# Kernel tuning notes

Hardware: AMD Instinct MI355X
Metric: run time of the kernel (lower is better)

## Reference

```python
import jax, jax.numpy as jnp
import numpy as np

N_NODES = 10000
N_EDGES = 160000
BN_EPS = 1e-5


def _sage(xx, src, dst, Wl, bl, Wr, n):
    # SAGEConv: lin_l(mean of in-neighbors) + lin_r(x)
    s = jax.ops.segment_sum(xx[src], dst, num_segments=n)
    cnt = jax.ops.segment_sum(jnp.ones((src.shape[0], 1), xx.dtype), dst, num_segments=n)
    mean = s / jnp.maximum(cnt, 1.0)
    return mean @ Wl + bl + xx @ Wr


def _gin(xx, src, dst, W1, b1, W2, b2, n):
    # GINConv (eps=0): MLP(x + sum of neighbors), MLP = Lin-ReLU-Lin-ReLU
    agg = xx + jax.ops.segment_sum(xx[src], dst, num_segments=n)
    h = jax.nn.relu(agg @ W1 + b1)
    return jax.nn.relu(h @ W2 + b2)


def _gat(xx, s2, d2, W, a_s, a_d, b, heads, ch, n):
    # GATConv with self-loops already appended in (s2, d2)
    h = (xx @ W).reshape(n, heads, ch)          # [N,H,C]
    al_s = (h * a_s).sum(-1)                     # [N,H]
    al_d = (h * a_d).sum(-1)                     # [N,H]
    e = jax.nn.leaky_relu(al_s[s2] + al_d[d2], negative_slope=0.2)  # [E',H]
    m = jax.ops.segment_max(e, d2, num_segments=n)
    ex = jnp.exp(e - m[d2])
    den = jax.ops.segment_sum(ex, d2, num_segments=n)
    coef = ex / den[d2]                          # segment softmax over dst
    out = jax.ops.segment_sum(h[s2] * coef[:, :, None], d2, num_segments=n)
    return out.reshape(n, heads * ch) + b


def reference(x, edge_index, train_edge_id,
              Wp1, bp1, Wp2, bp2, Wp3, bp3,
              sage1_Wl, sage1_bl, sage1_Wr, sage2_Wl, sage2_bl, sage2_Wr,
              gin1_W1, gin1_b1, gin1_W2, gin1_b2,
              gin2_W1, gin2_b1, gin2_W2, gin2_b2, gin_lin_W, gin_lin_b,
              gat1_W, gat1_as, gat1_ad, gat1_b,
              gat2_W, gat2_as, gat2_ad, gat2_b,
              fusion_w, lin1_W, lin1_b, lin2_W, lin2_b, fc2_W, fc2_b):
    n = x.shape[0]
    src, dst = edge_index[0], edge_index[1]
    # --- ppc: PointNet-style encoder: per-point MLP (16->64->128->256) + max pool over points ---
    pts = x[:, :, :16]                            # [N,L,16]
    h = jax.nn.relu(pts @ Wp1 + bp1)
    h = jax.nn.relu(h @ Wp2 + bp2)
    h = jax.nn.relu(h @ Wp3 + bp3)
    feat = h.max(axis=1)                          # [N,256]
    # --- SAGE branch ---
    hs = jax.nn.relu(_sage(feat, src, dst, sage1_Wl, sage1_bl, sage1_Wr, n))
    out_sage = _sage(hs, src, dst, sage2_Wl, sage2_bl, sage2_Wr, n)
    # --- GIN branch ---
    hg = jax.nn.relu(_gin(feat, src, dst, gin1_W1, gin1_b1, gin1_W2, gin1_b2, n))
    hg = jax.nn.relu(_gin(hg, src, dst, gin2_W1, gin2_b1, gin2_W2, gin2_b2, n))
    out_gin = hg @ gin_lin_W + gin_lin_b
    # --- GAT branch (self-loops per PyG default) ---
    loop = jnp.arange(n)
    s2 = jnp.concatenate([src, loop])
    d2 = jnp.concatenate([dst, loop])
    ha = jax.nn.relu(_gat(feat, s2, d2, gat1_W, gat1_as, gat1_ad, gat1_b, 8, 10, n))
    out_gat = _gat(ha, s2, d2, gat2_W, gat2_as, gat2_ad, gat2_b, 1, 512, n)
    # --- weighted fusion + batch norm (batch stats, no affine) ---
    y = fusion_w[0] * out_sage + fusion_w[1] * out_gin + fusion_w[2] * out_gat
    mu = y.mean(axis=0)
    var = y.var(axis=0)
    y = (y - mu) / jnp.sqrt(var + BN_EPS)
    # --- head ---
    y = jax.nn.relu(y @ lin1_W + lin1_b)
    y = y @ lin2_W + lin2_b
    # --- edge-pair gather + multiply for link scoring ---
    nid = edge_index[:, train_edge_id]            # [2,T]
    z = y[nid[0]] * y[nid[1]]
    return z @ fc2_W + fc2_b                      # [T,7]


def setup_inputs() -> dict:
    key = jax.random.key(0)
    ks = iter(jax.random.split(key, 64))
    def nrm(shape, s=0.02):
        return jax.random.normal(next(ks), shape, dtype=jnp.float32) * s
    inp = {}
    inp['x'] = jax.random.normal(next(ks), (N_NODES, 128, 16), dtype=jnp.float32)
    inp['edge_index'] = jax.random.randint(next(ks), (2, N_EDGES), 0, N_NODES, dtype=jnp.int32)
    inp['train_edge_id'] = jax.random.randint(next(ks), (50000,), 0, N_EDGES, dtype=jnp.int32)
    # ppc point encoder
    inp['Wp1'] = nrm((16, 64)); inp['bp1'] = nrm((64,))
    inp['Wp2'] = nrm((64, 128)); inp['bp2'] = nrm((128,))
    inp['Wp3'] = nrm((128, 256)); inp['bp3'] = nrm((256,))
    # SAGE: 256->128->512
    inp['sage1_Wl'] = nrm((256, 128)); inp['sage1_bl'] = nrm((128,)); inp['sage1_Wr'] = nrm((256, 128))
    inp['sage2_Wl'] = nrm((128, 512)); inp['sage2_bl'] = nrm((512,)); inp['sage2_Wr'] = nrm((128, 512))
    # GIN: 2 convs (256->128->128, 128->128->128) + lin 128->512
    inp['gin1_W1'] = nrm((256, 128)); inp['gin1_b1'] = nrm((128,))
    inp['gin1_W2'] = nrm((128, 128)); inp['gin1_b2'] = nrm((128,))
    inp['gin2_W1'] = nrm((128, 128)); inp['gin2_b1'] = nrm((128,))
    inp['gin2_W2'] = nrm((128, 128)); inp['gin2_b2'] = nrm((128,))
    inp['gin_lin_W'] = nrm((128, 512)); inp['gin_lin_b'] = nrm((512,))
    # GAT: layer1 256 -> 8 heads x 10 (concat=80), layer2 80 -> 512 (1 head)
    inp['gat1_W'] = nrm((256, 80)); inp['gat1_as'] = nrm((8, 10)); inp['gat1_ad'] = nrm((8, 10)); inp['gat1_b'] = nrm((80,))
    inp['gat2_W'] = nrm((80, 512)); inp['gat2_as'] = nrm((1, 512)); inp['gat2_ad'] = nrm((1, 512)); inp['gat2_b'] = nrm((512,))
    # fusion + head
    inp['fusion_w'] = jnp.ones((3,), jnp.float32)
    inp['lin1_W'] = nrm((512, 512)); inp['lin1_b'] = nrm((512,))
    inp['lin2_W'] = nrm((512, 512)); inp['lin2_b'] = nrm((512,))
    inp['fc2_W'] = nrm((512, 7)); inp['fc2_b'] = nrm((7,))
    return inp
```

## Files before the change

kernel.cpp:

```cpp
#include <hip/hip_runtime.h>
#include <math.h>

#define NN 10000
#define NE 160000
#define NT 50000

typedef unsigned short u16;
typedef unsigned int u32;
typedef __attribute__((ext_vector_type(8))) short bf16x8;
typedef __attribute__((ext_vector_type(4))) float f32x4;

__device__ __forceinline__ float bf2f(u16 u) { return __uint_as_float(((u32)u) << 16); }
__device__ __forceinline__ u16 f2bf(float f) {
    u32 x = __float_as_uint(f);
    return (u16)((x + 0x7fffu + ((x >> 16) & 1u)) >> 16);
}
__device__ __forceinline__ u32 cvtpk(float a, float b) {
    u32 r;
    asm("v_cvt_pk_bf16_f32 %0, %1, %2" : "=v"(r) : "v"(a), "v"(b));
    return r;
}
__device__ __forceinline__ float lrelu(float x) { return x > 0.f ? x : 0.2f * x; }

#define MFMA16(a, b, c) __builtin_amdgcn_mfma_f32_16x16x32_bf16((a), (b), (c), 0, 0, 0)

__global__ void k_wfrag(const float* __restrict__ W1, const float* __restrict__ W2,
                        const float* __restrict__ W3,
                        u16* __restrict__ W1f, u16* __restrict__ W2f, u16* __restrict__ W3f) {
    int i = blockIdx.x * 256 + threadIdx.x;
    if (i < 2048) {
        int e = i & 7, l = (i >> 3) & 63, nt = i >> 9;
        int k = (l >> 4) * 8 + e, c = nt * 16 + (l & 15);
        W1f[i] = (k < 16) ? f2bf(W1[k * 64 + c]) : (u16)0;
    }
    if (i < 8192) {
        int e = i & 7, l = (i >> 3) & 63, nt = (i >> 9) & 7, ks = i >> 12;
        int k = ks * 32 + (l >> 4) * 8 + e, c = nt * 16 + (l & 15);
        W2f[i] = f2bf(W2[k * 128 + c]);
    }
    if (i < 32768) {
        int e = i & 7, l = (i >> 3) & 63, nt = (i >> 9) & 15, ks = i >> 13;
        int k = ks * 32 + (l >> 4) * 8 + e, c = nt * 16 + (l & 15);
        W3f[i] = f2bf(W3[k * 256 + c]);
    }
}

__global__ void k_pack(const float* __restrict__ W, u16* __restrict__ Wf, int K, int Mt) {
    int total = (((K + 63) & ~63) >> 5) * Mt * 512;
    for (int i = blockIdx.x * 256 + threadIdx.x; i < total; i += gridDim.x * 256) {
        int e = i & 7, l = (i >> 3) & 63, mt = (i >> 9) % Mt, kk = i / (Mt << 9);
        int k = (kk << 5) + ((l >> 4) << 3) + e;
        int c = (mt << 4) + (l & 15);
        Wf[i] = (k < K) ? f2bf(W[(size_t)k * (Mt << 4) + c]) : (u16)0;
    }
}

__global__ __launch_bounds__(256) void k_pointnet_mfma(
    const float* __restrict__ x,
    const u16* __restrict__ W1f, const float* __restrict__ b1,
    const u16* __restrict__ W2f, const float* __restrict__ b2,
    const u16* __restrict__ W3f, const float* __restrict__ b3,
    u16* __restrict__ featb)
{
    __shared__ u16 buf[16384];

    const int node = blockIdx.x;
    const int t = threadIdx.x;
    const int w = t >> 6;
    const int l = t & 63;
    const int lr = l & 15;
    const int lg = l >> 4;

    {
        union { u32 q[4]; bf16x8 v; } ua0, ua1;
        ua0.q[0] = ua0.q[1] = ua0.q[2] = ua0.q[3] = 0;
        ua1 = ua0;
        if (lg < 2) {
            const float* px = x + ((size_t)node * 128 + w * 32 + lr) * 16 + lg * 8;
            float4 f0 = *(const float4*)px;
            float4 f1 = *(const float4*)(px + 4);
            ua0.q[0] = cvtpk(f0.x, f0.y); ua0.q[1] = cvtpk(f0.z, f0.w);
            ua0.q[2] = cvtpk(f1.x, f1.y); ua0.q[3] = cvtpk(f1.z, f1.w);
            float4 g0 = *(const float4*)(px + 256);
            float4 g1 = *(const float4*)(px + 260);
            ua1.q[0] = cvtpk(g0.x, g0.y); ua1.q[1] = cvtpk(g0.z, g0.w);
            ua1.q[2] = cvtpk(g1.x, g1.y); ua1.q[3] = cvtpk(g1.z, g1.w);
        }
        f32x4 acc[2][4];
        #pragma unroll
        for (int nt = 0; nt < 4; ++nt) {
            float bv = b1[nt * 16 + lr];
            f32x4 ci = {bv, bv, bv, bv};
            bf16x8 bf_ = *(const bf16x8*)(W1f + (nt * 64 + l) * 8);
            acc[0][nt] = MFMA16(ua0.v, bf_, ci);
            acc[1][nt] = MFMA16(ua1.v, bf_, ci);
        }
        #pragma unroll
        for (int mt = 0; mt < 2; ++mt) {
            #pragma unroll
            for (int nt = 0; nt < 4; ++nt) {
                int col = nt * 16 + lr;
                int r0 = w * 32 + mt * 16 + lg * 4;
                u32 p01 = cvtpk(fmaxf(acc[mt][nt][0], 0.f), fmaxf(acc[mt][nt][1], 0.f));
                u32 p23 = cvtpk(fmaxf(acc[mt][nt][2], 0.f), fmaxf(acc[mt][nt][3], 0.f));
                buf[((r0    ) * 64 + col) ^ (((r0    ) & 7) << 3)] = (u16)p01;
                buf[((r0 + 1) * 64 + col) ^ (((r0 + 1) & 7) << 3)] = (u16)(p01 >> 16);
                buf[((r0 + 2) * 64 + col) ^ (((r0 + 2) & 7) << 3)] = (u16)p23;
                buf[((r0 + 3) * 64 + col) ^ (((r0 + 3) & 7) << 3)] = (u16)(p23 >> 16);
            }
        }
    }

    {
        bf16x8 af[2][2];
        #pragma unroll
        for (int mt = 0; mt < 2; ++mt) {
            #pragma unroll
            for (int ks = 0; ks < 2; ++ks) {
                int row = w * 32 + mt * 16 + lr;
                int elem = row * 64 + ks * 32 + lg * 8;
                af[mt][ks] = *(const bf16x8*)&buf[elem ^ ((row & 7) << 3)];
            }
        }
        __syncthreads();

        f32x4 acc2[2][8];
        #pragma unroll
        for (int nt = 0; nt < 8; ++nt) {
            float bv = b2[nt * 16 + lr];
            f32x4 ci = {bv, bv, bv, bv};
            acc2[0][nt] = ci;
            acc2[1][nt] = ci;
        }
        #pragma unroll
        for (int ks = 0; ks < 2; ++ks) {
            #pragma unroll
            for (int nt = 0; nt < 8; ++nt) {
                bf16x8 bf_ = *(const bf16x8*)(W2f + ((ks * 8 + nt) * 64 + l) * 8);
                acc2[0][nt] = MFMA16(af[0][ks], bf_, acc2[0][nt]);
                acc2[1][nt] = MFMA16(af[1][ks], bf_, acc2[1][nt]);
            }
        }
        #pragma unroll
        for (int mt = 0; mt < 2; ++mt) {
            #pragma unroll
            for (int nt = 0; nt < 8; ++nt) {
                int col = nt * 16 + lr;
                int r0 = w * 32 + mt * 16 + lg * 4;
                u32 p01 = cvtpk(fmaxf(acc2[mt][nt][0], 0.f), fmaxf(acc2[mt][nt][1], 0.f));
                u32 p23 = cvtpk(fmaxf(acc2[mt][nt][2], 0.f), fmaxf(acc2[mt][nt][3], 0.f));
                buf[((r0    ) * 128 + col) ^ (((r0    ) & 7) << 3)] = (u16)p01;
                buf[((r0 + 1) * 128 + col) ^ (((r0 + 1) & 7) << 3)] = (u16)(p01 >> 16);
                buf[((r0 + 2) * 128 + col) ^ (((r0 + 2) & 7) << 3)] = (u16)p23;
                buf[((r0 + 3) * 128 + col) ^ (((r0 + 3) & 7) << 3)] = (u16)(p23 >> 16);
            }
        }
    }
    __syncthreads();

    {
        float pmax[4] = {0.f, 0.f, 0.f, 0.f};
        #pragma unroll
        for (int half = 0; half < 2; ++half) {
            f32x4 acc3[4][4];
            #pragma unroll
            for (int nt = 0; nt < 4; ++nt) {
                float bv = b3[w * 64 + nt * 16 + lr];
                f32x4 ci = {bv, bv, bv, bv};
                #pragma unroll
                for (int mt = 0; mt < 4; ++mt) acc3[mt][nt] = ci;
            }
            #pragma unroll
            for (int ks = 0; ks < 4; ++ks) {
                bf16x8 bf_[4];
                #pragma unroll
                for (int nt = 0; nt < 4; ++nt)
                    bf_[nt] = *(const bf16x8*)(W3f + ((ks * 16 + w * 4 + nt) * 64 + l) * 8);
                #pragma unroll
                for (int mt = 0; mt < 4; ++mt) {
                    int row = half * 64 + mt * 16 + lr;
                    int elem = row * 128 + ks * 32 + lg * 8;
                    bf16x8 af = *(const bf16x8*)&buf[elem ^ ((row & 7) << 3)];
                    #pragma unroll
                    for (int nt = 0; nt < 4; ++nt)
                        acc3[mt][nt] = MFMA16(af, bf_[nt], acc3[mt][nt]);
                }
            }
            #pragma unroll
            for (int nt = 0; nt < 4; ++nt) {
                #pragma unroll
                for (int mt = 0; mt < 4; ++mt) {
                    pmax[nt] = fmaxf(fmaxf(pmax[nt], acc3[mt][nt][0]),
                                     fmaxf(acc3[mt][nt][1],
                                           fmaxf(acc3[mt][nt][2], acc3[mt][nt][3])));
                }
            }
        }
        #pragma unroll
        for (int nt = 0; nt < 4; ++nt) {
            pmax[nt] = fmaxf(pmax[nt], __shfl_xor(pmax[nt], 16));
            pmax[nt] = fmaxf(pmax[nt], __shfl_xor(pmax[nt], 32));
        }
        if (l < 16) {
            #pragma unroll
            for (int nt = 0; nt < 4; ++nt)
                featb[(size_t)node * 256 + w * 64 + nt * 16 + l] = f2bf(pmax[nt]);
        }
    }
}

template<int CT, int DUAL, int RELU, int OUTM, int NORMA>
__global__ __launch_bounds__(256) void k_mm(
    const u16* __restrict__ A, const u16* __restrict__ A2,
    const u16* __restrict__ Bf, const u16* __restrict__ B2f,
    const float* __restrict__ bias, int K, int Mt,
    void* __restrict__ outp,
    const float* __restrict__ scale_ptr, int scale_idx,
    const float* __restrict__ mu, const float* __restrict__ inv)
{
    __shared__ u16 As[8192];
    __shared__ u16 As2[DUAL ? 8192 : 8];

    const int t = threadIdx.x;
    const int l = t & 63, lr = l & 15, lg = l >> 4;
    const int row0 = blockIdx.y << 7;
    const int ct0 = blockIdx.x * CT;
    const int m0 = (t >> 6) << 5;

    f32x4 acc[2][CT];
    #pragma unroll
    for (int nt = 0; nt < CT; ++nt) {
        float bv = bias ? bias[((ct0 + nt) << 4) + lr] : 0.f;
        f32x4 ci = {bv, bv, bv, bv};
        acc[0][nt] = ci;
        acc[1][nt] = ci;
    }

    const int KS = (K + 63) >> 6;
    for (int kblk = 0; kblk < KS; ++kblk) {
        const int k0 = kblk << 6;
        if (kblk) __syncthreads();
        #pragma unroll
        for (int j = 0; j < 4; ++j) {
            int si = t + (j << 8);
            int row = si >> 3, seg = si & 7;
            int gr = row0 + row;
            int kb = k0 + (seg << 3);
            int soff = ((row << 6) + (seg << 3)) ^ ((row & 7) << 3);
            if (NORMA) {
                u32 q0 = 0, q1 = 0, q2 = 0, q3 = 0;
                if (gr < NN) {
                    const float* Af = (const float*)A;
                    float4 f0 = *(const float4*)(Af + (size_t)gr * K + kb);
                    float4 f1 = *(const float4*)(Af + (size_t)gr * K + kb + 4);
                    q0 = cvtpk((f0.x - mu[kb+0]) * inv[kb+0], (f0.y - mu[kb+1]) * inv[kb+1]);
                    q1 = cvtpk((f0.z - mu[kb+2]) * inv[kb+2], (f0.w - mu[kb+3]) * inv[kb+3]);
                    q2 = cvtpk((f1.x - mu[kb+4]) * inv[kb+4], (f1.y - mu[kb+5]) * inv[kb+5]);
                    q3 = cvtpk((f1.z - mu[kb+6]) * inv[kb+6], (f1.w - mu[kb+7]) * inv[kb+7]);
                }
                u32* dst = (u32*)&As[soff];
                dst[0] = q0; dst[1] = q1; dst[2] = q2; dst[3] = q3;
            } else {
                bf16x8 v = {0,0,0,0,0,0,0,0};
                bf16x8 v2 = {0,0,0,0,0,0,0,0};
                if (gr < NN) {
                    if (kb + 8 <= K) {
                        v = *(const bf16x8*)(A + (size_t)gr * K + kb);
                        if (DUAL) v2 = *(const bf16x8*)(A2 + (size_t)gr * K + kb);
                    } else {
                        #pragma unroll
                        for (int e = 0; e < 8; ++e) if (kb + e < K) {
                            v[e] = (short)A[(size_t)gr * K + kb + e];
                            if (DUAL) v2[e] = (short)A2[(size_t)gr * K + kb + e];
                        }
                    }
                }
                *(bf16x8*)&As[soff] = v;
                if (DUAL) *(bf16x8*)&As2[soff] = v2;
            }
        }
        __syncthreads();
        #pragma unroll
        for (int ks = 0; ks < 2; ++ks) {
            const int kk = (k0 >> 5) + ks;
            bf16x8 bfr[CT];
            #pragma unroll
            for (int nt = 0; nt < CT; ++nt)
                bfr[nt] = *(const bf16x8*)(Bf + (((size_t)kk * Mt + ct0 + nt) << 9) + (l << 3));
            #pragma unroll
            for (int mt = 0; mt < 2; ++mt) {
                int row = m0 + (mt << 4) + lr;
                int soff = ((row << 6) + (ks << 5) + (lg << 3)) ^ ((row & 7) << 3);
                bf16x8 af = *(const bf16x8*)&As[soff];
                #pragma unroll
                for (int nt = 0; nt < CT; ++nt)
                    acc[mt][nt] = MFMA16(af, bfr[nt], acc[mt][nt]);
            }
            if (DUAL) {
                bf16x8 bfr2[CT];
                #pragma unroll
                for (int nt = 0; nt < CT; ++nt)
                    bfr2[nt] = *(const bf16x8*)(B2f + (((size_t)kk * Mt + ct0 + nt) << 9) + (l << 3));
                #pragma unroll
                for (int mt = 0; mt < 2; ++mt) {
                    int row = m0 + (mt << 4) + lr;
                    int soff = ((row << 6) + (ks << 5) + (lg << 3)) ^ ((row & 7) << 3);
                    bf16x8 af2 = *(const bf16x8*)&As2[soff];
                    #pragma unroll
                    for (int nt = 0; nt < CT; ++nt)
                        acc[mt][nt] = MFMA16(af2, bfr2[nt], acc[mt][nt]);
                }
            }
        }
    }

    float scale = 1.f;
    if (OUTM == 1 || OUTM == 2) scale = scale_ptr[scale_idx];
    const int M = Mt << 4;
    #pragma unroll
    for (int mt = 0; mt < 2; ++mt) {
        #pragma unroll
        for (int nt = 0; nt < CT; ++nt) {
            int col = ((ct0 + nt) << 4) + lr;
            #pragma unroll
            for (int r = 0; r < 4; ++r) {
                int grow = row0 + m0 + (mt << 4) + (lg << 2) + r;
                if (grow >= NN) continue;
                float v = acc[mt][nt][r];
                if (RELU) v = fmaxf(v, 0.f);
                size_t o = (size_t)grow * M + col;
                if (OUTM == 0) ((u16*)outp)[o] = f2bf(v);
                else if (OUTM == 1) ((float*)outp)[o] = scale * v;
                else if (OUTM == 2) ((float*)outp)[o] += scale * v;
                else ((float*)outp)[o] = v;
            }
        }
    }
}

__global__ void k_init(int* counts, float* s1, float* s2) {
    int i = blockIdx.x * 256 + threadIdx.x;
    if (i < NN) counts[i] = 0;
    if (i < 512) { s1[i] = 0.f; s2[i] = 0.f; }
}

__global__ void k_csr_count(const int* __restrict__ EI, int* counts) {
    int e = blockIdx.x * 256 + threadIdx.x;
    if (e < NE) atomicAdd(&counts[EI[NE + e]], 1);
}

__global__ __launch_bounds__(1024) void k_scan(const int* __restrict__ counts,
                                               int* offs, int* cursor) {
    __shared__ int buf[1024];
    int t = threadIdx.x;
    int carry = 0;
    for (int chunk = 0; chunk < (NN + 1023) / 1024; ++chunk) {
        int i = chunk * 1024 + t;
        int v = (i < NN) ? counts[i] : 0;
        buf[t] = v;
        __syncthreads();
        for (int o = 1; o < 1024; o <<= 1) {
            int xv = (t >= o) ? buf[t - o] : 0;
            __syncthreads();
            buf[t] += xv;
            __syncthreads();
        }
        int excl = buf[t] - v;
        if (i < NN) { offs[i] = carry + excl; cursor[i] = carry + excl; }
        carry += buf[1023];
        __syncthreads();
    }
    if (t == 0) offs[NN] = carry;
}

__global__ void k_csr_scatter(const int* __restrict__ EI, int* cursor, int* csrc) {
    int e = blockIdx.x * 256 + threadIdx.x;
    if (e < NE) {
        int d = EI[NE + e];
        int pos = atomicAdd(&cursor[d], 1);
        csrc[pos] = EI[e];
    }
}

template<int WU, int MODE>
__global__ void k_aggb(const u32* __restrict__ in, u32* __restrict__ out,
                       const int* __restrict__ offs, const int* __restrict__ srcs)
{
    int node = blockIdx.x;
    int c = threadIdx.x;
    int o0 = offs[node], o1 = offs[node + 1];
    float s0 = 0.f, s1 = 0.f;
    for (int j = o0; j < o1; ++j) {
        u32 v = in[(size_t)srcs[j] * WU + c];
        s0 += bf2f((u16)(v & 0xffff));
        s1 += bf2f((u16)(v >> 16));
    }
    if (MODE == 0) {
        int d = o1 - o0;
        float r = 1.f / (float)(d > 0 ? d : 1);
        s0 *= r; s1 *= r;
    } else {
        u32 v = in[(size_t)node * WU + c];
        s0 += bf2f((u16)(v & 0xffff));
        s1 += bf2f((u16)(v >> 16));
    }
    out[(size_t)node * WU + c] = cvtpk(s0, s1);
}

__global__ void k_gat1_al(const u16* __restrict__ h, const float* __restrict__ a_s,
                          const float* __restrict__ a_d, float* als, float* ald) {
    int idx = blockIdx.x * 64 + threadIdx.x;
    if (idx >= NN * 8) return;
    int node = idx >> 3, hh = idx & 7;
    float s = 0.f, d = 0.f;
    #pragma unroll
    for (int c = 0; c < 10; ++c) {
        float hv = bf2f(h[node * 80 + hh * 10 + c]);
        s = fmaf(hv, a_s[hh * 10 + c], s);
        d = fmaf(hv, a_d[hh * 10 + c], d);
    }
    als[idx] = s; ald[idx] = d;
}

__global__ __launch_bounds__(128) void k_gat1_attn(
    const u16* __restrict__ h, const float* __restrict__ als,
    const float* __restrict__ ald, const float* __restrict__ bias,
    const int* __restrict__ offs, const int* __restrict__ srcs,
    u16* __restrict__ ha)
{
    int node = blockIdx.x;
    int t = threadIdx.x;
    if (t >= 80) return;
    int hh = t / 10;
    int o0 = offs[node], o1 = offs[node + 1];
    float ad = ald[node * 8 + hh];
    float eself = lrelu(als[node * 8 + hh] + ad);
    float m = eself;
    for (int j = o0; j < o1; ++j)
        m = fmaxf(m, lrelu(als[srcs[j] * 8 + hh] + ad));
    float den = 0.f, num = 0.f;
    {
        float wgt = __expf(eself - m);
        den += wgt; num += wgt * bf2f(h[(size_t)node * 80 + t]);
    }
    for (int j = o0; j < o1; ++j) {
        int sc = srcs[j];
        float wgt = __expf(lrelu(als[sc * 8 + hh] + ad) - m);
        den += wgt; num += wgt * bf2f(h[(size_t)sc * 80 + t]);
    }
    ha[(size_t)node * 80 + t] = f2bf(fmaxf(num / den + bias[t], 0.f));
}

__global__ __launch_bounds__(256) void k_gat2_al(
    const u16* __restrict__ h, const float* __restrict__ a_s,
    const float* __restrict__ a_d, float* als, float* ald)
{
    __shared__ float rs[256], rd[256];
    int node = blockIdx.x, t = threadIdx.x;
    float h0 = bf2f(h[(size_t)node * 512 + t]);
    float h1 = bf2f(h[(size_t)node * 512 + 256 + t]);
    rs[t] = h0 * a_s[t] + h1 * a_s[256 + t];
    rd[t] = h0 * a_d[t] + h1 * a_d[256 + t];
    __syncthreads();
    for (int o = 128; o > 0; o >>= 1) {
        if (t < o) { rs[t] += rs[t + o]; rd[t] += rd[t + o]; }
        __syncthreads();
    }
    if (t == 0) { als[node] = rs[0]; ald[node] = rd[0]; }
}

__global__ __launch_bounds__(256) void k_gat2_attn(
    const u16* __restrict__ h, const float* __restrict__ als,
    const float* __restrict__ ald, const float* __restrict__ bias,
    const int* __restrict__ offs, const int* __restrict__ srcs,
    const float* __restrict__ fusion_w, float* __restrict__ Y)
{
    int node = blockIdx.x;
    int t = threadIdx.x;
    float w2 = fusion_w[2];
    int o0 = offs[node], o1 = offs[node + 1];
    float ad = ald[node];
    float eself = lrelu(als[node] + ad);
    float m = eself;
    for (int j = o0; j < o1; ++j) m = fmaxf(m, lrelu(als[srcs[j]] + ad));
    float den = 0.f, n0 = 0.f, n1 = 0.f;
    {
        float wgt = __expf(eself - m);
        den += wgt;
        n0 += wgt * bf2f(h[(size_t)node * 512 + t]);
        n1 += wgt * bf2f(h[(size_t)node * 512 + 256 + t]);
    }
    for (int j = o0; j < o1; ++j) {
        int sc = srcs[j];
        float wgt = __expf(lrelu(als[sc] + ad) - m);
        den += wgt;
        n0 += wgt * bf2f(h[(size_t)sc * 512 + t]);
        n1 += wgt * bf2f(h[(size_t)sc * 512 + 256 + t]);
    }
    Y[(size_t)node * 512 + t]       += w2 * (n0 / den + bias[t]);
    Y[(size_t)node * 512 + 256 + t] += w2 * (n1 / den + bias[256 + t]);
}

__global__ __launch_bounds__(256) void k_bn_stats(const float* __restrict__ Y,
                                                  float* ssum, float* ssq) {
    int t = threadIdx.x;
    int b = blockIdx.x;
    int r0 = b * 40, r1 = r0 + 40;
    if (r1 > NN) r1 = NN;
    float s0 = 0, s1 = 0, q0 = 0, q1 = 0;
    for (int r = r0; r < r1; ++r) {
        float v0 = Y[(size_t)r * 512 + t];
        float v1 = Y[(size_t)r * 512 + 256 + t];
        s0 += v0; q0 += v0 * v0; s1 += v1; q1 += v1 * v1;
    }
    atomicAdd(&ssum[t], s0); atomicAdd(&ssum[256 + t], s1);
    atomicAdd(&ssq[t], q0);  atomicAdd(&ssq[256 + t], q1);
}

__global__ void k_bn_final(const float* ssum, const float* ssq, float* mu, float* inv) {
    int c = blockIdx.x * 256 + threadIdx.x;
    if (c < 512) {
        float m = ssum[c] / (float)NN;
        float v = ssq[c] / (float)NN - m * m;
        mu[c] = m;
        inv[c] = rsqrtf(v + 1e-5f);
    }
}

__global__ __launch_bounds__(256) void k_final(
    const float* __restrict__ y2, const int* __restrict__ EI,
    const int* __restrict__ tid, const float* __restrict__ fcW,
    const float* __restrict__ fcb, float* __restrict__ out)
{
    int pair = blockIdx.x * 4 + (threadIdx.x >> 6);
    int lane = threadIdx.x & 63;
    if (pair >= NT) return;
    int eid = tid[pair];
    int a = EI[eid], b = EI[NE + eid];
    float acc[7] = {};
    for (int c = lane; c < 512; c += 64) {
        float v = y2[(size_t)a * 512 + c] * y2[(size_t)b * 512 + c];
        #pragma unroll
        for (int j = 0; j < 7; ++j) acc[j] = fmaf(v, fcW[c * 7 + j], acc[j]);
    }
    for (int o = 32; o > 0; o >>= 1) {
        #pragma unroll
        for (int j = 0; j < 7; ++j) acc[j] += __shfl_down(acc[j], o);
    }
    if (lane == 0) {
        #pragma unroll
        for (int j = 0; j < 7; ++j) out[(size_t)pair * 7 + j] = acc[j] + fcb[j];
    }
}

extern "C" void kernel_launch(void* const* d_in, const int* in_sizes, int n_in,
                              void* d_out, int out_size, void* d_ws, size_t ws_size,
                              hipStream_t stream)
{
    (void)in_sizes; (void)n_in; (void)out_size; (void)ws_size;
    const float* x        = (const float*)d_in[0];
    const int*   EI       = (const int*)d_in[1];
    const int*   tid      = (const int*)d_in[2];
    const float* Wp1      = (const float*)d_in[3];
    const float* bp1      = (const float*)d_in[4];
    const float* Wp2      = (const float*)d_in[5];
    const float* bp2      = (const float*)d_in[6];
    const float* Wp3      = (const float*)d_in[7];
    const float* bp3      = (const float*)d_in[8];
    const float* sage1_Wl = (const float*)d_in[9];
    const float* sage1_bl = (const float*)d_in[10];
    const float* sage1_Wr = (const float*)d_in[11];
    const float* sage2_Wl = (const float*)d_in[12];
    const float* sage2_bl = (const float*)d_in[13];
    const float* sage2_Wr = (const float*)d_in[14];
    const float* gin1_W1  = (const float*)d_in[15];
    const float* gin1_b1  = (const float*)d_in[16];
    const float* gin1_W2  = (const float*)d_in[17];
    const float* gin1_b2  = (const float*)d_in[18];
    const float* gin2_W1  = (const float*)d_in[19];
    const float* gin2_b1  = (const float*)d_in[20];
    const float* gin2_W2  = (const float*)d_in[21];
    const float* gin2_b2  = (const float*)d_in[22];
    const float* gin_lin_W= (const float*)d_in[23];
    const float* gin_lin_b= (const float*)d_in[24];
    const float* gat1_W   = (const float*)d_in[25];
    const float* gat1_as  = (const float*)d_in[26];
    const float* gat1_ad  = (const float*)d_in[27];
    const float* gat1_b   = (const float*)d_in[28];
    const float* gat2_W   = (const float*)d_in[29];
    const float* gat2_as  = (const float*)d_in[30];
    const float* gat2_ad  = (const float*)d_in[31];
    const float* gat2_b   = (const float*)d_in[32];
    const float* fusion_w = (const float*)d_in[33];
    const float* lin1_W   = (const float*)d_in[34];
    const float* lin1_b   = (const float*)d_in[35];
    const float* lin2_W   = (const float*)d_in[36];
    const float* lin2_b   = (const float*)d_in[37];
    const float* fc2_W    = (const float*)d_in[38];
    const float* fc2_b    = (const float*)d_in[39];

    char* base = (char*)d_ws;
    u16* mean1 = (u16*)base;
    u16* agg1  = (u16*)(base + 5120000);
    u16* h2b   = (u16*)base;
    u16* y1b   = (u16*)(base + 20480000);
    float* y2  = (float*)base;
    size_t off = 40960000;
    u16* featb = (u16*)(base + off); off += 5120000;
    u16* hsb   = (u16*)(base + off); off += 2560000;
    u16* mean2 = (u16*)(base + off); off += 2560000;
    u16* g1    = (u16*)(base + off); off += 2560000;
    u16* g2    = (u16*)(base + off); off += 2560000;
    u16* hgat  = (u16*)(base + off); off += 1600000;
    u16* hab   = (u16*)(base + off); off += 1600000;
    float* Y   = (float*)(base + off); off += 20480000;
    float* als1 = (float*)(base + off); off += 320000;
    float* ald1 = (float*)(base + off); off += 320000;
    float* als2 = (float*)(base + off); off += 40000;
    float* ald2 = (float*)(base + off); off += 40000;
    float* ssum = (float*)(base + off); off += 2048;
    float* ssq  = (float*)(base + off); off += 2048;
    float* mu   = (float*)(base + off); off += 2048;
    float* inv  = (float*)(base + off); off += 2048;
    int* counts = (int*)(base + off); off += 40000;
    int* offs   = (int*)(base + off); off += 40016;
    int* cursor = (int*)(base + off); off += 40000;
    int* csrc   = (int*)(base + off); off += 640000;
    u16* W1f    = (u16*)(base + off); off += 4096;
    u16* W2f    = (u16*)(base + off); off += 16384;
    u16* W3f    = (u16*)(base + off); off += 65536;
    u16* s1lf   = (u16*)(base + off); off += 65536;
    u16* s1rf   = (u16*)(base + off); off += 65536;
    u16* g1w1f  = (u16*)(base + off); off += 65536;
    u16* g1w2f  = (u16*)(base + off); off += 32768;
    u16* ga1f   = (u16*)(base + off); off += 40960;
    u16* s2lf   = (u16*)(base + off); off += 131072;
    u16* s2rf   = (u16*)(base + off); off += 131072;
    u16* g2w1f  = (u16*)(base + off); off += 32768;
    u16* g2w2f  = (u16*)(base + off); off += 32768;
    u16* glinf  = (u16*)(base + off); off += 131072;
    u16* ga2f   = (u16*)(base + off); off += 131072;
    u16* l1f    = (u16*)(base + off); off += 524288;
    u16* l2f    = (u16*)(base + off); off += 524288;

    k_init<<<40, 256, 0, stream>>>(counts, ssum, ssq);
    k_wfrag<<<128, 256, 0, stream>>>(Wp1, Wp2, Wp3, W1f, W2f, W3f);
    k_pack<<<256, 256, 0, stream>>>(sage1_Wl, s1lf, 256, 8);
    k_pack<<<256, 256, 0, stream>>>(sage1_Wr, s1rf, 256, 8);
    k_pack<<<256, 256, 0, stream>>>(gin1_W1,  g1w1f, 256, 8);
    k_pack<<<256, 256, 0, stream>>>(gin1_W2,  g1w2f, 128, 8);
    k_pack<<<256, 256, 0, stream>>>(gat1_W,   ga1f, 256, 5);
    k_pack<<<256, 256, 0, stream>>>(sage2_Wl, s2lf, 128, 32);
    k_pack<<<256, 256, 0, stream>>>(sage2_Wr, s2rf, 128, 32);
    k_pack<<<256, 256, 0, stream>>>(gin2_W1,  g2w1f, 128, 8);
    k_pack<<<256, 256, 0, stream>>>(gin2_W2,  g2w2f, 128, 8);
    k_pack<<<256, 256, 0, stream>>>(gin_lin_W, glinf, 128, 32);
    k_pack<<<256, 256, 0, stream>>>(gat2_W,   ga2f, 80, 32);
    k_pack<<<256, 256, 0, stream>>>(lin1_W,   l1f, 512, 32);
    k_pack<<<256, 256, 0, stream>>>(lin2_W,   l2f, 512, 32);

    k_pointnet_mfma<<<NN, 256, 0, stream>>>(x, W1f, bp1, W2f, bp2, W3f, bp3, featb);
    k_csr_count<<<(NE + 255) / 256, 256, 0, stream>>>(EI, counts);
    k_scan<<<1, 1024, 0, stream>>>(counts, offs, cursor);
    k_csr_scatter<<<(NE + 255) / 256, 256, 0, stream>>>(EI, cursor, csrc);

    dim3 gN128(4, 79), gN80(5, 79), gWide(4, 79);

    k_aggb<128, 0><<<NN, 128, 0, stream>>>((const u32*)featb, (u32*)mean1, offs, csrc);
    k_aggb<128, 1><<<NN, 128, 0, stream>>>((const u32*)featb, (u32*)agg1, offs, csrc);

    k_mm<2,1,1,0,0><<<gN128, 256, 0, stream>>>(mean1, featb, s1lf, s1rf, sage1_bl,
                                               256, 8, hsb, nullptr, 0, nullptr, nullptr);
    k_mm<2,0,1,0,0><<<gN128, 256, 0, stream>>>(agg1, nullptr, g1w1f, nullptr, gin1_b1,
                                               256, 8, g1, nullptr, 0, nullptr, nullptr);
    k_mm<2,0,1,0,0><<<gN128, 256, 0, stream>>>(g1, nullptr, g1w2f, nullptr, gin1_b2,
                                               128, 8, g2, nullptr, 0, nullptr, nullptr);
    k_mm<1,0,0,0,0><<<gN80, 256, 0, stream>>>(featb, nullptr, ga1f, nullptr, nullptr,
                                              256, 5, hgat, nullptr, 0, nullptr, nullptr);
    k_gat1_al<<<1250, 64, 0, stream>>>(hgat, gat1_as, gat1_ad, als1, ald1);
    k_gat1_attn<<<NN, 128, 0, stream>>>(hgat, als1, ald1, gat1_b, offs, csrc, hab);

    k_aggb<64, 0><<<NN, 64, 0, stream>>>((const u32*)hsb, (u32*)mean2, offs, csrc);
    k_mm<8,1,0,1,0><<<gWide, 256, 0, stream>>>(mean2, hsb, s2lf, s2rf, sage2_bl,
                                               128, 32, Y, fusion_w, 0, nullptr, nullptr);
    k_aggb<64, 1><<<NN, 64, 0, stream>>>((const u32*)g2, (u32*)g1, offs, csrc);
    k_mm<2,0,1,0,0><<<gN128, 256, 0, stream>>>(g1, nullptr, g2w1f, nullptr, gin2_b1,
                                               128, 8, g2, nullptr, 0, nullptr, nullptr);
    k_mm<2,0,1,0,0><<<gN128, 256, 0, stream>>>(g2, nullptr, g2w2f, nullptr, gin2_b2,
                                               128, 8, g1, nullptr, 0, nullptr, nullptr);
    k_mm<8,0,0,2,0><<<gWide, 256, 0, stream>>>(g1, nullptr, glinf, nullptr, gin_lin_b,
                                               128, 32, Y, fusion_w, 1, nullptr, nullptr);
    k_mm<8,0,0,0,0><<<gWide, 256, 0, stream>>>(hab, nullptr, ga2f, nullptr, nullptr,
                                               80, 32, h2b, nullptr, 0, nullptr, nullptr);
    k_gat2_al<<<NN, 256, 0, stream>>>(h2b, gat2_as, gat2_ad, als2, ald2);
    k_gat2_attn<<<NN, 256, 0, stream>>>(h2b, als2, ald2, gat2_b, offs, csrc, fusion_w, Y);

    k_bn_stats<<<250, 256, 0, stream>>>(Y, ssum, ssq);
    k_bn_final<<<2, 256, 0, stream>>>(ssum, ssq, mu, inv);
    k_mm<8,0,1,0,1><<<gWide, 256, 0, stream>>>((const u16*)Y, nullptr, l1f, nullptr, lin1_b,
                                               512, 32, y1b, nullptr, 0, mu, inv);
    k_mm<8,0,0,3,0><<<gWide, 256, 0, stream>>>(y1b, nullptr, l2f, nullptr, lin2_b,
                                               512, 32, y2, nullptr, 0, nullptr, nullptr);

    k_final<<<(NT + 3) / 4, 256, 0, stream>>>(y2, EI, tid, fc2_W, fc2_b, (float*)d_out);
}
```

Baseline: 601.8 us.

## Compute transposed PointNet layers to pass layer-1 output via shuffles, not LDS

Swaps the MFMA operand order for the first two PointNet layers so each lane holds channel-major results. The layer-1 activations now reach layer 2 through lane shuffles in registers, which removes the LDS write, the LDS read and the barrier between those layers. The layer-2 output is written to shared memory with packed 8-byte stores instead of scalar 16-bit stores. In exchange it adds shuffle instructions and more register pressure, and the changed lane mapping is a correctness risk.

```diff
diff --git a/kernel.cpp b/kernel.cpp
--- a/kernel.cpp
+++ b/kernel.cpp
@@ -62,7 +62,7 @@
     const u16* __restrict__ W3f, const float* __restrict__ b3,
     u16* __restrict__ featb)
 {
-    __shared__ u16 buf[16384];
+    __shared__ __align__(16) u16 buf[16384];
 
     const int node = blockIdx.x;
     const int t = threadIdx.x;
@@ -71,88 +71,73 @@
     const int lr = l & 15;
     const int lg = l >> 4;
 
+    u32 pk1[4][2][2];
     {
-        union { u32 q[4]; bf16x8 v; } ua0, ua1;
-        ua0.q[0] = ua0.q[1] = ua0.q[2] = ua0.q[3] = 0;
-        ua1 = ua0;
+        union { u32 q[4]; bf16x8 v; } xb0, xb1;
+        xb0.q[0] = xb0.q[1] = xb0.q[2] = xb0.q[3] = 0;
+        xb1 = xb0;
         if (lg < 2) {
             const float* px = x + ((size_t)node * 128 + w * 32 + lr) * 16 + lg * 8;
             float4 f0 = *(const float4*)px;
             float4 f1 = *(const float4*)(px + 4);
-            ua0.q[0] = cvtpk(f0.x, f0.y); ua0.q[1] = cvtpk(f0.z, f0.w);
-            ua0.q[2] = cvtpk(f1.x, f1.y); ua0.q[3] = cvtpk(f1.z, f1.w);
+            xb0.q[0] = cvtpk(f0.x, f0.y); xb0.q[1] = cvtpk(f0.z, f0.w);
+            xb0.q[2] = cvtpk(f1.x, f1.y); xb0.q[3] = cvtpk(f1.z, f1.w);
             float4 g0 = *(const float4*)(px + 256);
             float4 g1 = *(const float4*)(px + 260);
-            ua1.q[0] = cvtpk(g0.x, g0.y); ua1.q[1] = cvtpk(g0.z, g0.w);
-            ua1.q[2] = cvtpk(g1.x, g1.y); ua1.q[3] = cvtpk(g1.z, g1.w);
-        }
-        f32x4 acc[2][4];
-        #pragma unroll
-        for (int nt = 0; nt < 4; ++nt) {
-            float bv = b1[nt * 16 + lr];
-            f32x4 ci = {bv, bv, bv, bv};
-            bf16x8 bf_ = *(const bf16x8*)(W1f + (nt * 64 + l) * 8);
-            acc[0][nt] = MFMA16(ua0.v, bf_, ci);
-            acc[1][nt] = MFMA16(ua1.v, bf_, ci);
-        }
-        #pragma unroll
-        for (int mt = 0; mt < 2; ++mt) {
-            #pragma unroll
-            for (int nt = 0; nt < 4; ++nt) {
-                int col = nt * 16 + lr;
-                int r0 = w * 32 + mt * 16 + lg * 4;
-                u32 p01 = cvtpk(fmaxf(acc[mt][nt][0], 0.f), fmaxf(acc[mt][nt][1], 0.f));
-                u32 p23 = cvtpk(fmaxf(acc[mt][nt][2], 0.f), fmaxf(acc[mt][nt][3], 0.f));
-                buf[((r0    ) * 64 + col) ^ (((r0    ) & 7) << 3)] = (u16)p01;
-                buf[((r0 + 1) * 64 + col) ^ (((r0 + 1) & 7) << 3)] = (u16)(p01 >> 16);
-                buf[((r0 + 2) * 64 + col) ^ (((r0 + 2) & 7) << 3)] = (u16)p23;
-                buf[((r0 + 3) * 64 + col) ^ (((r0 + 3) & 7) << 3)] = (u16)(p23 >> 16);
-            }
+            xb1.q[0] = cvtpk(g0.x, g0.y); xb1.q[1] = cvtpk(g0.z, g0.w);
+            xb1.q[2] = cvtpk(g1.x, g1.y); xb1.q[3] = cvtpk(g1.z, g1.w);
+        }
+        #pragma unroll
+        for (int cht = 0; cht < 4; ++cht) {
+            f32x4 ci = *(const f32x4*)(b1 + cht * 16 + 4 * lg);
+            bf16x8 wf = *(const bf16x8*)(W1f + (cht * 64 + l) * 8);
+            f32x4 a0 = MFMA16(wf, xb0.v, ci);
+            f32x4 a1 = MFMA16(wf, xb1.v, ci);
+            pk1[cht][0][0] = cvtpk(fmaxf(a0[0], 0.f), fmaxf(a0[1], 0.f));
+            pk1[cht][0][1] = cvtpk(fmaxf(a0[2], 0.f), fmaxf(a0[3], 0.f));
+            pk1[cht][1][0] = cvtpk(fmaxf(a1[0], 0.f), fmaxf(a1[1], 0.f));
+            pk1[cht][1][1] = cvtpk(fmaxf(a1[2], 0.f), fmaxf(a1[3], 0.f));
         }
     }
 
     {
-        bf16x8 af[2][2];
-        #pragma unroll
-        for (int mt = 0; mt < 2; ++mt) {
-            #pragma unroll
-            for (int ks = 0; ks < 2; ++ks) {
-                int row = w * 32 + mt * 16 + lr;
-                int elem = row * 64 + ks * 32 + lg * 8;
-                af[mt][ks] = *(const bf16x8*)&buf[elem ^ ((row & 7) << 3)];
-            }
-        }
-        __syncthreads();
-
-        f32x4 acc2[2][8];
-        #pragma unroll
-        for (int nt = 0; nt < 8; ++nt) {
-            float bv = b2[nt * 16 + lr];
-            f32x4 ci = {bv, bv, bv, bv};
-            acc2[0][nt] = ci;
-            acc2[1][nt] = ci;
+        f32x4 acc2[8][2];
+        #pragma unroll
+        for (int mt = 0; mt < 8; ++mt) {
+            f32x4 ci = *(const f32x4*)(b2 + mt * 16 + 4 * lg);
+            acc2[mt][0] = ci;
+            acc2[mt][1] = ci;
         }
         #pragma unroll
         for (int ks = 0; ks < 2; ++ks) {
-            #pragma unroll
-            for (int nt = 0; nt < 8; ++nt) {
-                bf16x8 bf_ = *(const bf16x8*)(W2f + ((ks * 8 + nt) * 64 + l) * 8);
-                acc2[0][nt] = MFMA16(af[0][ks], bf_, acc2[0][nt]);
-                acc2[1][nt] = MFMA16(af[1][ks], bf_, acc2[1][nt]);
-            }
-        }
-        #pragma unroll
-        for (int mt = 0; mt < 2; ++mt) {
-            #pragma unroll
-            for (int nt = 0; nt < 8; ++nt) {
-                int col = nt * 16 + lr;
-                int r0 = w * 32 + mt * 16 + lg * 4;
-                u32 p01 = cvtpk(fmaxf(acc2[mt][nt][0], 0.f), fmaxf(acc2[mt][nt][1], 0.f));
-                u32 p23 = cvtpk(fmaxf(acc2[mt][nt][2], 0.f), fmaxf(acc2[mt][nt][3], 0.f));
-                buf[((r0    ) * 128 + col) ^ (((r0    ) & 7) << 3)] = (u16)p01;
-                buf[((r0 + 1) * 128 + col) ^ (((r0 + 1) & 7) << 3)] = (u16)(p01 >> 16);
-                buf[((r0 + 2) * 128 + col) ^ (((r0 + 2) & 7) << 3)] = (u16)p23;
-                buf[((r0 + 3) * 128 + col) ^ (((r0 + 3) & 7) << 3)] = (u16)(p23 >> 16);
+            union { u32 q[4]; bf16x8 v; } B2[2];
+            #pragma unroll
+            for (int ptt = 0; ptt < 2; ++ptt) {
+                #pragma unroll
+                for (int j = 0; j < 4; ++j) {
+                    int s = ((2 * (lg & 1) + (j >> 1)) << 4) + lr;
+                    int lo = __shfl((int)pk1[2 * ks][ptt][j & 1], s);
+                    int hi = __shfl((int)pk1[2 * ks + 1][ptt][j & 1], s);
+                    B2[ptt].q[j] = (u32)((lg >> 1) ? hi : lo);
+                }
+            }
+            #pragma unroll
+            for (int mt = 0; mt < 8; ++mt) {
+                bf16x8 af = *(const bf16x8*)(W2f + ((ks * 8 + mt) * 64 + l) * 8);
+                acc2[mt][0] = MFMA16(af, B2[0].v, acc2[mt][0]);
+                acc2[mt][1] = MFMA16(af, B2[1].v, acc2[mt][1]);
+            }
+        }
+        #pragma unroll
+        for (int mt = 0; mt < 8; ++mt) {
+            #pragma unroll
+            for (int ptt = 0; ptt < 2; ++ptt) {
+                int pt = w * 32 + ptt * 16 + lr;
+                int ch0 = mt * 16 + 4 * lg;
+                u32 q0 = cvtpk(fmaxf(acc2[mt][ptt][0], 0.f), fmaxf(acc2[mt][ptt][1], 0.f));
+                u32 q1 = cvtpk(fmaxf(acc2[mt][ptt][2], 0.f), fmaxf(acc2[mt][ptt][3], 0.f));
+                int idx = (pt * 128 + ch0) ^ ((pt & 7) << 3);
+                *(uint2*)&buf[idx] = make_uint2(q0, q1);
             }
         }
     }
```

Measured after the change: 593.7 us. About the same (-1.3%).
